# Kernel optimization log

Measured on AMD Instinct MI355X. Metric: run time of the kernel, lower is better.

The kernel has to match this reference:

```python
import jax, jax.numpy as jnp
import numpy as np
import math

K = 3          # wavelet order
ALPHA = 5      # fourier modes
LLEV = 0       # coarsest level
CVAL = 1       # channel multiplicity
K2 = K * K     # 9
B, NX, NY, T = 8, 64, 64, 64


def _linear(x, w, b):
    # torch nn.Linear: y = x @ W^T + b, W is [out, in]
    return jnp.einsum('...i,oi->...o', x, w) + b


def _wavelet_transform(x, ec_d, ec_s):
    # strided 4-way gather + concat along channel, then small matmuls
    xa = jnp.concatenate([x[:, ::2, ::2], x[:, ::2, 1::2],
                          x[:, 1::2, ::2], x[:, 1::2, 1::2]], axis=-1)
    return jnp.matmul(xa, ec_d), jnp.matmul(xa, ec_s)


def _even_odd(x, rc_ee, rc_eo, rc_oe, rc_oo):
    b, nx, ny, t, c, ich = x.shape
    k2 = ich // 2
    x_ee = jnp.matmul(x, rc_ee)
    x_eo = jnp.matmul(x, rc_eo)
    x_oe = jnp.matmul(x, rc_oe)
    x_oo = jnp.matmul(x, rc_oo)
    # interleave along Ny then Nx (equivalent to strided scatter into zeros)
    e = jnp.stack([x_ee, x_eo], axis=3).reshape(b, nx, 2 * ny, t, c, k2)
    o = jnp.stack([x_oe, x_oo], axis=3).reshape(b, nx, 2 * ny, t, c, k2)
    return jnp.stack([e, o], axis=2).reshape(b, 2 * nx, 2 * ny, t, c, k2)


def _kernel_ft(x, w1, w2, w3, w4, lo_w, lo_b):
    # sparseKernelFT3d
    b, nx, ny, t, c, ich = x.shape
    xr = x.reshape(b, nx, ny, t, c * ich).transpose(0, 4, 1, 2, 3)  # [B,C,Nx,Ny,T]
    xf = jnp.fft.rfftn(xr, axes=(-3, -2, -1))
    m = ALPHA
    l1 = min(m, nx // 2 + 1)
    l2 = min(m, ny // 2 + 1)
    cm = lambda a, w: jnp.einsum('bixyz,ioxyz->boxyz', a, w)
    w1c = w1[..., 0] + 1j * w1[..., 1]
    w2c = w2[..., 0] + 1j * w2[..., 1]
    w3c = w3[..., 0] + 1j * w3[..., 1]
    w4c = w4[..., 0] + 1j * w4[..., 1]
    out = jnp.zeros((b, c * ich, nx, ny, t // 2 + 1), dtype=xf.dtype)
    out = out.at[:, :, :l1, :l2, :m].set(cm(xf[:, :, :l1, :l2, :m], w1c[:, :, :l1, :l2, :]))
    out = out.at[:, :, nx - l1:, :l2, :m].set(cm(xf[:, :, nx - l1:, :l2, :m], w2c[:, :, :l1, :l2, :]))
    out = out.at[:, :, :l1, ny - l2:, :m].set(cm(xf[:, :, :l1, ny - l2:, :m], w3c[:, :, :l1, :l2, :]))
    out = out.at[:, :, nx - l1:, ny - l2:, :m].set(cm(xf[:, :, nx - l1:, ny - l2:, :m], w4c[:, :, :l1, :l2, :]))
    y = jnp.fft.irfftn(out, s=(nx, ny, t), axes=(-3, -2, -1))
    y = jax.nn.relu(y.transpose(0, 2, 3, 4, 1))
    y = _linear(y, lo_w, lo_b)
    return y.reshape(b, nx, ny, t, c, ich)


def _kernel_conv(x, cw, cb, lw, lb):
    # sparseKernel3d: conv3d(3,1,1) + ReLU, then Linear
    b, nx, ny, t, c, ich = x.shape
    xr = x.reshape(b, nx, ny, t, c * ich).transpose(0, 4, 1, 2, 3)
    y = jax.lax.conv_general_dilated(xr, cw, (1, 1, 1), 'SAME',
                                     dimension_numbers=('NCDHW', 'OIDHW', 'NCDHW'))
    y = jax.nn.relu(y + cb[None, :, None, None, None])
    y = _linear(y.transpose(0, 2, 3, 4, 1), lw, lb)
    return y.reshape(b, nx, ny, t, c, ich)


def setup_inputs() -> dict:
    key = jax.random.key(0)
    ks = jax.random.split(key, 24)
    r = lambda i, shp, s: jax.random.normal(ks[i], shp, dtype=jnp.float32) * s
    return {
        'x': r(0, (B, NX, NY, T, CVAL, K2), 1.0),
        'ec_s': r(1, (4 * K2, K2), 0.2), 'ec_d': r(2, (4 * K2, K2), 0.2),
        'rc_ee': r(3, (2 * K2, K2), 0.25), 'rc_eo': r(4, (2 * K2, K2), 0.25),
        'rc_oe': r(5, (2 * K2, K2), 0.25), 'rc_oo': r(6, (2 * K2, K2), 0.25),
        'w1': r(7, (K2, K2, ALPHA, ALPHA, ALPHA, 2), 0.05),
        'w2': r(8, (K2, K2, ALPHA, ALPHA, ALPHA, 2), 0.05),
        'w3': r(9, (K2, K2, ALPHA, ALPHA, ALPHA, 2), 0.05),
        'w4': r(10, (K2, K2, ALPHA, ALPHA, ALPHA, 2), 0.05),
        'A_Lo_w': r(11, (K2, K2), 0.2), 'A_Lo_b': r(12, (K2,), 0.1),
        'B_conv_w': r(13, (K2, K2, 3, 3, 3), 0.06), 'B_conv_b': r(14, (K2,), 0.1),
        'B_Lo_w': r(15, (K2, K2), 0.2), 'B_Lo_b': r(16, (K2,), 0.1),
        'C_conv_w': r(17, (K2, K2, 3, 3, 3), 0.06), 'C_conv_b': r(18, (K2,), 0.1),
        'C_Lo_w': r(19, (K2, K2), 0.2), 'C_Lo_b': r(20, (K2,), 0.1),
        'T0_w': r(21, (K2, K2), 0.2), 'T0_b': r(22, (K2,), 0.1),
    }


def reference(x, ec_s, ec_d, rc_ee, rc_eo, rc_oe, rc_oo, w1, w2, w3, w4,
              A_Lo_w, A_Lo_b, B_conv_w, B_conv_b, B_Lo_w, B_Lo_b,
              C_conv_w, C_conv_b, C_Lo_w, C_Lo_b, T0_w, T0_b):
    b, nx, ny, t, c, ich = x.shape
    ns = int(math.floor(math.log2(nx)))
    Ud, Us = [], []
    for _ in range(ns - LLEV):  # decompose
        d, x = _wavelet_transform(x, ec_d, ec_s)
        Ud.append(_kernel_ft(d, w1, w2, w3, w4, A_Lo_w, A_Lo_b)
                  + _kernel_conv(x, B_conv_w, B_conv_b, B_Lo_w, B_Lo_b))
        Us.append(_kernel_conv(d, C_conv_w, C_conv_b, C_Lo_w, C_Lo_b))
    n0 = 2 ** LLEV
    x = _linear(x.reshape(b, n0, n0, t, c * ich), T0_w, T0_b)
    x = x.reshape(b, n0, n0, t, c, ich)
    for i in range(ns - 1 - LLEV, -1, -1):  # reconstruct
        x = x + Us[i]
        x = jnp.concatenate([x, Ud[i]], axis=-1)
        x = _even_odd(x, rc_ee, rc_eo, rc_oe, rc_oo)
    return x
```

## Files before the change

kernel.cpp:

```cpp
#include <hip/hip_runtime.h>

#define TWO_PI 6.283185307179586f

struct Meta {
    int bz[7], by[7], bxm[7], bix[7], biz[7], bcv[7];
    int n[6], l1[6], L[6], NT[6];
    int soff[6];
    int tAo[6], tBo[6], tDo[6];
};

__device__ __forceinline__ int find_lev(const int* pre) {
    int lev = 0;
    #pragma unroll
    for (int i = 1; i < 6; ++i) lev += (int)(blockIdx.x >= (unsigned)pre[i]);
    return lev;
}


__global__ void wavelet_kernel(const float* __restrict__ x,
                               float* __restrict__ d, float* __restrict__ s,
                               const float* __restrict__ ec_d,
                               const float* __restrict__ ec_s,
                               int n, int total, int aos_in)
{
    __shared__ float wd[324], wsm[324];
    for (int i = threadIdx.x; i < 324; i += blockDim.x) { wd[i] = ec_d[i]; wsm[i] = ec_s[i]; }
    __syncthreads();
    int idx = blockIdx.x * blockDim.x + threadIdx.x;
    if (idx >= total) return;
    int it = idx & 63; int tmp = idx >> 6;
    int iy = tmp % n; tmp /= n;
    int ix = tmp % n; int b = tmp / n;
    int n2 = 2 * n;
    float a[36];
    if (aos_in) {
        const float* base = x + ((((size_t)(b * n2 + 2 * ix) * n2 + 2 * iy) * 64 + it) * 9);
        const float* p0 = base;
        const float* p1 = base + 576;
        const float* p2 = base + (size_t)n2 * 576;
        const float* p3 = p2 + 576;
        #pragma unroll
        for (int k = 0; k < 9; ++k) { a[k] = p0[k]; a[9+k] = p1[k]; a[18+k] = p2[k]; a[27+k] = p3[k]; }
    } else {
        const float* base = x + ((size_t)(b * n2 + 2 * ix) * n2 + 2 * iy) * 576 + it;
        const float* p0 = base;
        const float* p1 = base + 576;
        const float* p2 = base + (size_t)n2 * 576;
        const float* p3 = p2 + 576;
        #pragma unroll
        for (int k = 0; k < 9; ++k) { a[k] = p0[k*64]; a[9+k] = p1[k*64]; a[18+k] = p2[k*64]; a[27+k] = p3[k*64]; }
    }
    size_t ob = (size_t)(idx >> 6) * 576 + it;
    #pragma unroll
    for (int oc = 0; oc < 9; ++oc) {
        float vd = 0.f, vs = 0.f;
        #pragma unroll
        for (int k = 0; k < 36; ++k) { vd += a[k] * wd[k*9+oc]; vs += a[k] * wsm[k*9+oc]; }
        d[ob + oc*64] = vd; s[ob + oc*64] = vs;
    }
}

__global__ __launch_bounds__(256, 2)
void conv2_kernel(const float* __restrict__ s_all, float* __restrict__ ud_all,
                  const float* __restrict__ d_all, float* __restrict__ us_all,
                  const float* __restrict__ Bcw, const float* __restrict__ Bcb,
                  const float* __restrict__ Blw, const float* __restrict__ Blb,
                  const float* __restrict__ Ccw, const float* __restrict__ Ccb,
                  const float* __restrict__ Clw, const float* __restrict__ Clb,
                  Meta m)
{
    const int which = blockIdx.y;
    const float* cw = which ? Ccw : Bcw;
    const float* cb = which ? Ccb : Bcb;
    const float* lw = which ? Clw : Blw;
    const float* lb = which ? Clb : Blb;

    __shared__ float scw2[2430];
    __shared__ float slw[81], scb[9], slb[9];
    for (int i = threadIdx.x; i < 2187; i += 256) {
        int wo = i / 81, rem = i % 81, o = rem / 9, ic = rem % 9;
        scw2[(wo * 9 + o) * 10 + ic] = cw[(o * 9 + ic) * 27 + wo];
    }
    if (threadIdx.x < 81) slw[threadIdx.x] = lw[threadIdx.x];
    if (threadIdx.x < 9) { scb[threadIdx.x] = cb[threadIdx.x]; slb[threadIdx.x] = lb[threadIdx.x]; }
    __syncthreads();

    int lev = find_lev(m.bcv);
    int n = m.n[lev];
    int idx = (blockIdx.x - m.bcv[lev]) * 256 + threadIdx.x;
    int nh = (n + 1) >> 1;
    int total = 8 * n * nh * 64;
    if (idx >= total) return;
    int t = idx & 63; int tmp = idx >> 6;
    int iy0 = (tmp % nh) * 2; tmp /= nh;
    int ix = tmp % n; int b = tmp / n;
    bool has1 = (iy0 + 1) < n;
    const float* in = (which ? d_all : s_all) + (size_t)m.soff[lev] * 576;
    float* out      = (which ? us_all : ud_all) + (size_t)m.soff[lev] * 576;

    float acc0[9], acc1[9];
    #pragma unroll
    for (int o = 0; o < 9; ++o) { acc0[o] = scb[o]; acc1[o] = scb[o]; }

    for (int dd = 0; dd < 9; ++dd) {
        int dx = dd / 3 - 1, dt = dd % 3 - 1;
        int jx = ix + dx, jt = t + dt;
        bool okxt = ((unsigned)jx < (unsigned)n) && ((unsigned)jt < 64u);
        const float* rowbase = in + ((size_t)(b * n + (okxt ? jx : 0)) * n) * 576
                                  + (okxt ? jt : 0);
        float va[9], vb[9];
        {
            int jy = iy0 - 1; bool ok = okxt && (jy >= 0);
            const float* p = rowbase + (size_t)(ok ? jy : 0) * 576;
            #pragma unroll
            for (int ic = 0; ic < 9; ++ic) va[ic] = ok ? p[ic*64] : 0.f;
            const float* q = rowbase + (size_t)iy0 * 576;
            #pragma unroll
            for (int ic = 0; ic < 9; ++ic) vb[ic] = okxt ? q[ic*64] : 0.f;
        }
        #pragma unroll
        for (int k = 0; k < 3; ++k) {
            const float* wbase = &scw2[(((dx + 1) * 3 + k) * 3 + (dt + 1)) * 90];
            #pragma unroll
            for (int o = 0; o < 9; ++o) {
                const float* wp = wbase + o * 10;
                float2 w01 = *(const float2*)(wp);
                float2 w23 = *(const float2*)(wp + 2);
                float2 w45 = *(const float2*)(wp + 4);
                float2 w67 = *(const float2*)(wp + 6);
                float  w8  = wp[8];
                acc0[o] += va[0]*w01.x + va[1]*w01.y + va[2]*w23.x + va[3]*w23.y
                         + va[4]*w45.x + va[5]*w45.y + va[6]*w67.x + va[7]*w67.y + va[8]*w8;
                acc1[o] += vb[0]*w01.x + vb[1]*w01.y + vb[2]*w23.x + vb[3]*w23.y
                         + vb[4]*w45.x + vb[5]*w45.y + vb[6]*w67.x + vb[7]*w67.y + vb[8]*w8;
            }
            if (k < 2) {
                int jy = iy0 + k + 1; bool ok = okxt && (jy < n);
                const float* p = rowbase + (size_t)(ok ? jy : 0) * 576;
                #pragma unroll
                for (int ic = 0; ic < 9; ++ic) { va[ic] = vb[ic]; vb[ic] = ok ? p[ic*64] : 0.f; }
            }
        }
    }
    {
        float r[9];
        #pragma unroll
        for (int o = 0; o < 9; ++o) r[o] = fmaxf(acc0[o], 0.f);
        size_t ob = (size_t)((b * n + ix) * n + iy0) * 576 + t;
        #pragma unroll
        for (int o2 = 0; o2 < 9; ++o2) {
            float vv = slb[o2];
            #pragma unroll
            for (int o = 0; o < 9; ++o) vv += r[o] * slw[o2 * 9 + o];
            if (which == 0) out[ob + o2*64] += vv; else out[ob + o2*64] = vv;
        }
    }
    if (has1) {
        float r[9];
        #pragma unroll
        for (int o = 0; o < 9; ++o) r[o] = fmaxf(acc1[o], 0.f);
        size_t ob = (size_t)((b * n + ix) * n + iy0 + 1) * 576 + t;
        #pragma unroll
        for (int o2 = 0; o2 < 9; ++o2) {
            float vv = slb[o2];
            #pragma unroll
            for (int o = 0; o < 9; ++o) vv += r[o] * slw[o2 * 9 + o];
            if (which == 0) out[ob + o2*64] += vv; else out[ob + o2*64] = vv;
        }
    }
}

__global__ void fwdz_kernel(const float* __restrict__ d_all, float2* __restrict__ tA, Meta m)
{
    int lev = find_lev(m.bz);
    int n = m.n[lev];
    int idx = (blockIdx.x - m.bz[lev]) * 256 + threadIdx.x;
    int total = 8 * n * n * 45;
    if (idx >= total) return;
    int ic = idx % 9; int tmp = idx / 9;
    int kz = tmp % 5; int site = tmp / 5;
    const float* p = d_all + (size_t)(m.soff[lev] + site) * 576 + ic * 64;
    float re = 0.f, im = 0.f;
    for (int it = 0; it < 64; ++it) {
        int mm = (kz * it) & 63;
        float sv, cv; __sincosf((TWO_PI / 64.0f) * mm, &sv, &cv);
        float v = p[it];
        re += v * cv; im -= v * sv;
    }
    tA[m.tAo[lev] + idx] = make_float2(re, im);
}

__global__ void fwdy_kernel(const float2* __restrict__ tA, float2* __restrict__ tB, Meta m)
{
    int lev = find_lev(m.by);
    int n = m.n[lev], l1 = m.l1[lev], L = m.L[lev];
    int idx = (blockIdx.x - m.by[lev]) * 256 + threadIdx.x;
    int total = 8 * n * L * 45;
    if (idx >= total) return;
    int c45 = idx % 45; int tmp = idx / 45;
    int kyI = tmp % L; tmp /= L;
    int ix = tmp % n; int b = tmp / n;
    int ky = (kyI < l1) ? kyI : (n - L + kyI);
    const float2* p = tA + m.tAo[lev] + ((size_t)(b * n + ix) * n) * 45 + c45;
    float re = 0.f, im = 0.f;
    for (int iy = 0; iy < n; ++iy) {
        int mm = (ky * iy) & (n - 1);
        float sv, cv; __sincosf((TWO_PI / n) * mm, &sv, &cv);
        float2 a = p[(size_t)iy * 45];
        re += a.x * cv + a.y * sv;
        im += a.y * cv - a.x * sv;
    }
    tB[m.tBo[lev] + idx] = make_float2(re, im);
}

__global__ void fwdxmix_kernel(const float2* __restrict__ tB, float2* __restrict__ tD,
                               const float* __restrict__ w1, const float* __restrict__ w2,
                               const float* __restrict__ w3, const float* __restrict__ w4,
                               Meta m)
{
    __shared__ float2 sFzy[32 * 45];
    __shared__ float2 sF[10 * 45];
    int lev = find_lev(m.bxm);
    int n = m.n[lev], l1 = m.l1[lev], L = m.L[lev];
    int lb = blockIdx.x - m.bxm[lev];
    int kyI = lb % L;
    int b   = lb / L;
    int ky = (kyI < l1) ? kyI : (n - L + kyI);
    int nload = n * 45;
    for (int i = threadIdx.x; i < nload; i += blockDim.x) {
        int ix = i / 45, c = i % 45;
        sFzy[i] = tB[m.tBo[lev] + ((size_t)(b * n + ix) * L + kyI) * 45 + c];
    }
    __syncthreads();
    int nf = L * 45;
    for (int i = threadIdx.x; i < nf; i += blockDim.x) {
        int kxI = i / 45, c = i % 45;
        int kx = (kxI < l1) ? kxI : (n - L + kxI);
        float re = 0.f, im = 0.f;
        for (int ix = 0; ix < n; ++ix) {
            int mm = (kx * ix) & (n - 1);
            float sv, cv; __sincosf((TWO_PI / n) * mm, &sv, &cv);
            float2 a = sFzy[ix * 45 + c];
            re += a.x * cv + a.y * sv;
            im += a.y * cv - a.x * sv;
        }
        sF[i] = make_float2(re, im);
    }
    __syncthreads();
    bool ly = ky < l1, hy = ky >= n - l1;
    for (int i = threadIdx.x; i < nf; i += blockDim.x) {
        int kxI = i / 45, c = i % 45;
        int kz = c / 9, oc = c % 9;
        int kx = (kxI < l1) ? kxI : (n - L + kxI);
        bool lx = kx < l1, hx = kx >= n - l1;
        const float* w; int wx, wy;
        if (hx && hy)      { w = w4; wx = kx - (n - l1); wy = ky - (n - l1); }
        else if (lx && hy) { w = w3; wx = kx;            wy = ky - (n - l1); }
        else if (hx && ly) { w = w2; wx = kx - (n - l1); wy = ky; }
        else               { w = w1; wx = kx;            wy = ky; }
        const float* wb = w + (((size_t)oc * 5 + wx) * 5 + wy) * 10 + kz * 2;
        const float2* pf = &sF[kxI * 45 + kz * 9];
        float re = 0.f, im = 0.f;
        #pragma unroll
        for (int ic = 0; ic < 9; ++ic) {
            float2 a = pf[ic];
            float wr = wb[(size_t)ic * 2250];
            float wi = wb[(size_t)ic * 2250 + 1];
            re += a.x * wr - a.y * wi;
            im += a.x * wi + a.y * wr;
        }
        tD[m.tDo[lev] + (((size_t)(b * L + kxI) * L + kyI) * 5 + kz) * 9 + oc] = make_float2(re, im);
    }
}

__global__ void invx_kernel(const float2* __restrict__ tD, float2* __restrict__ tB, Meta m)
{
    int lev = find_lev(m.bix);
    int n = m.n[lev], l1 = m.l1[lev], L = m.L[lev];
    int idx = (blockIdx.x - m.bix[lev]) * 256 + threadIdx.x;
    int total = 8 * n * L * 45;
    if (idx >= total) return;
    int c45 = idx % 45; int tmp = idx / 45;
    int kyI = tmp % L; tmp /= L;
    int ix = tmp % n; int b = tmp / n;
    const float2* p = tD + m.tDo[lev] + ((size_t)b * L * L) * 45 + (size_t)kyI * 45 + c45;
    float re = 0.f, im = 0.f;
    for (int kxI = 0; kxI < L; ++kxI) {
        int kx = (kxI < l1) ? kxI : (n - L + kxI);
        int mm = (kx * ix) & (n - 1);
        float sv, cv; __sincosf((TWO_PI / n) * mm, &sv, &cv);
        float2 a = p[(size_t)kxI * L * 45];
        re += a.x * cv - a.y * sv;
        im += a.x * sv + a.y * cv;
    }
    tB[m.tBo[lev] + idx] = make_float2(re, im);
}

__global__ void invyz_kernel(const float2* __restrict__ tB, float* __restrict__ ud_all,
                             const float* __restrict__ lw, const float* __restrict__ lb,
                             Meta m)
{
    __shared__ float2 sG1[10 * 45];
    __shared__ float2 sG2[4 * 45];
    __shared__ float slw[81], slb[9];
    int lev = find_lev(m.biz);
    int n = m.n[lev], l1 = m.l1[lev], L = m.L[lev], NT = m.NT[lev];
    int TY = n / NT;
    int lb2 = blockIdx.x - m.biz[lev];
    int iyt = lb2 % NT;
    int ix  = (lb2 / NT) % n;
    int b   = lb2 / (NT * n);
    int iy0 = iyt * TY;
    if (threadIdx.x < 81) slw[threadIdx.x] = lw[threadIdx.x];
    if (threadIdx.x < 9)  slb[threadIdx.x] = lb[threadIdx.x];
    int nload = L * 45;
    for (int i = threadIdx.x; i < nload; i += blockDim.x)
        sG1[i] = tB[m.tBo[lev] + ((size_t)(b * n + ix) * L) * 45 + i];
    __syncthreads();
    int nf = TY * 45;
    for (int i = threadIdx.x; i < nf; i += blockDim.x) {
        int il = i / 45, c = i % 45;
        int iy = iy0 + il;
        float re = 0.f, im = 0.f;
        for (int kyI = 0; kyI < L; ++kyI) {
            int ky = (kyI < l1) ? kyI : (n - L + kyI);
            int mm = (ky * iy) & (n - 1);
            float sv, cv; __sincosf((TWO_PI / n) * mm, &sv, &cv);
            float2 a = sG1[kyI * 45 + c];
            re += a.x * cv - a.y * sv;
            im += a.x * sv + a.y * cv;
        }
        sG2[i] = make_float2(re, im);
    }
    __syncthreads();
    int t = threadIdx.x;
    if (t < TY * 64) {
        int il = t >> 6, it = t & 63;
        float inv_norm = 1.0f / ((float)n * (float)n * 64.0f);
        float cvz[5], svz[5];
        #pragma unroll
        for (int kz = 0; kz < 5; ++kz) {
            int mm = (kz * it) & 63;
            __sincosf((TWO_PI / 64.0f) * mm, &svz[kz], &cvz[kz]);
        }
        const float2* pg = &sG2[il * 45];
        float y[9];
        #pragma unroll
        for (int oc = 0; oc < 9; ++oc) {
            float v = 0.f;
            #pragma unroll
            for (int kz = 0; kz < 5; ++kz) {
                float2 a = pg[kz * 9 + oc];
                float term = a.x * cvz[kz] - a.y * svz[kz];
                v += (kz == 0 ? 1.0f : 2.0f) * term;
            }
            y[oc] = fmaxf(v * inv_norm, 0.f);
        }
        size_t ob = (size_t)(m.soff[lev] + (b * n + ix) * n + iy0 + il) * 576 + it;
        #pragma unroll
        for (int o2 = 0; o2 < 9; ++o2) {
            float v = slb[o2];
            #pragma unroll
            for (int oc = 0; oc < 9; ++oc) v += y[oc] * slw[o2 * 9 + oc];
            ud_all[ob + o2*64] = v;
        }
    }
}

__global__ void recon_kernel(const float* __restrict__ x, const float* __restrict__ Us,
                             const float* __restrict__ Ud, float* __restrict__ out,
                             const float* __restrict__ ree, const float* __restrict__ reo,
                             const float* __restrict__ roe, const float* __restrict__ roo,
                             const float* __restrict__ t0w, const float* __restrict__ t0b,
                             int n, int total, int apply_t0, int aos_out)
{
    __shared__ float s_m[4][162];
    __shared__ float st0[81], st0b[9];
    for (int i = threadIdx.x; i < 162; i += blockDim.x) {
        s_m[0][i] = ree[i]; s_m[1][i] = reo[i]; s_m[2][i] = roe[i]; s_m[3][i] = roo[i];
    }
    if (threadIdx.x < 81) st0[threadIdx.x] = t0w[threadIdx.x];
    if (threadIdx.x < 9)  st0b[threadIdx.x] = t0b[threadIdx.x];
    __syncthreads();
    int idx = blockIdx.x * blockDim.x + threadIdx.x;
    if (idx >= total) return;
    int it = idx & 63; int tmp = idx >> 6;
    int iy = tmp % n; tmp /= n;
    int ix = tmp % n; int b = tmp / n;
    float v[18];
    size_t ib = (size_t)(idx >> 6) * 576 + it;
    if (apply_t0) {
        float xr[9];
        #pragma unroll
        for (int k = 0; k < 9; ++k) xr[k] = x[ib + k*64];
        #pragma unroll
        for (int o = 0; o < 9; ++o) {
            float r = st0b[o];
            #pragma unroll
            for (int i = 0; i < 9; ++i) r += xr[i] * st0[o*9+i];
            v[o] = r + Us[ib + o*64];
        }
    } else {
        #pragma unroll
        for (int k = 0; k < 9; ++k) v[k] = x[ib + k*64] + Us[ib + k*64];
    }
    #pragma unroll
    for (int k = 0; k < 9; ++k) v[9+k] = Ud[ib + k*64];
    int n2 = 2 * n;
    #pragma unroll
    for (int q = 0; q < 4; ++q) {
        int rx = q >> 1, ry = q & 1;
        size_t site2 = ((size_t)(b * n2 + 2*ix + rx) * n2) + 2*iy + ry;
        const float* mm = s_m[q];
        if (aos_out) {
            size_t ob = (site2 * 64 + it) * 9;
            #pragma unroll
            for (int oc = 0; oc < 9; ++oc) {
                float r = 0.f;
                #pragma unroll
                for (int k = 0; k < 18; ++k) r += v[k] * mm[k*9+oc];
                out[ob + oc] = r;
            }
        } else {
            size_t ob = site2 * 576 + it;
            #pragma unroll
            for (int oc = 0; oc < 9; ++oc) {
                float r = 0.f;
                #pragma unroll
                for (int k = 0; k < 18; ++k) r += v[k] * mm[k*9+oc];
                out[ob + oc*64] = r;
            }
        }
    }
}

extern "C" void kernel_launch(void* const* d_in, const int* in_sizes, int n_in,
                              void* d_out, int out_size, void* d_ws, size_t ws_size,
                              hipStream_t stream)
{
    const float* x0    = (const float*)d_in[0];
    const float* ec_s  = (const float*)d_in[1];
    const float* ec_d  = (const float*)d_in[2];
    const float* rc_ee = (const float*)d_in[3];
    const float* rc_eo = (const float*)d_in[4];
    const float* rc_oe = (const float*)d_in[5];
    const float* rc_oo = (const float*)d_in[6];
    const float* w1    = (const float*)d_in[7];
    const float* w2    = (const float*)d_in[8];
    const float* w3    = (const float*)d_in[9];
    const float* w4    = (const float*)d_in[10];
    const float* A_Lo_w = (const float*)d_in[11];
    const float* A_Lo_b = (const float*)d_in[12];
    const float* B_cw  = (const float*)d_in[13];
    const float* B_cb  = (const float*)d_in[14];
    const float* B_lw  = (const float*)d_in[15];
    const float* B_lb  = (const float*)d_in[16];
    const float* C_cw  = (const float*)d_in[17];
    const float* C_cb  = (const float*)d_in[18];
    const float* C_lw  = (const float*)d_in[19];
    const float* C_lb  = (const float*)d_in[20];
    const float* T0_w  = (const float*)d_in[21];
    const float* T0_b  = (const float*)d_in[22];

    Meta m;
    int ns_[6] = {32, 16, 8, 4, 2, 1};
    int az = 0, ay = 0, axm = 0, aix = 0, aiz = 0, acv = 0;
    int aS = 0, aA = 0, aB = 0, aD = 0;
    for (int l = 0; l < 6; ++l) {
        int n = ns_[l];
        int l1 = (n / 2 + 1 < 5) ? (n / 2 + 1) : 5;
        int L = (2 * l1 < n) ? 2 * l1 : n;
        int TY = (n < 4) ? n : 4;
        int NT = n / TY;
        int nh = (n + 1) / 2;
        m.n[l] = n; m.l1[l] = l1; m.L[l] = L; m.NT[l] = NT;
        m.soff[l] = aS; m.tAo[l] = aA; m.tBo[l] = aB; m.tDo[l] = aD;
        m.bz[l] = az; m.by[l] = ay; m.bxm[l] = axm; m.bix[l] = aix; m.biz[l] = aiz; m.bcv[l] = acv;
        az  += (8 * n * n * 45 + 255) / 256;
        ay  += (8 * n * L * 45 + 255) / 256;
        axm += 8 * L;
        aix += (8 * n * L * 45 + 255) / 256;
        aiz += 8 * n * NT;
        acv += (8 * n * nh * 64 + 255) / 256;
        aS += 8 * n * n; aA += 8 * n * n * 45; aB += 8 * n * L * 45; aD += 8 * L * L * 45;
    }
    m.bz[6] = az; m.by[6] = ay; m.bxm[6] = axm; m.bix[6] = aix; m.biz[6] = aiz; m.bcv[6] = acv;

    float* ws = (float*)d_ws;
    size_t off = 0;
    auto alloc = [&](size_t nf) { float* p = ws + off; off += (nf + 3) & ~(size_t)3; return p; };
    size_t NSf = (size_t)aS * 576;
    float* d_all  = alloc(NSf);
    float* s_all  = alloc(NSf);
    float* ud_all = alloc(NSf);
    float* us_all = alloc(NSf);
    float2* tA = (float2*)alloc((size_t)aA * 2);
    float2* tB = (float2*)alloc((size_t)aB * 2);
    float2* tD = (float2*)alloc((size_t)aD * 2);
    float* pingA = alloc((size_t)8 * 32 * 32 * 64 * 9);
    float* pingB = alloc((size_t)8 * 16 * 16 * 64 * 9);

    const int BLK = 256;

    for (int lev = 0; lev < 6; ++lev) {
        int n = ns_[lev];
        const float* xin = (lev == 0) ? x0 : (s_all + (size_t)m.soff[lev-1] * 576);
        int total = 8 * n * n * 64;
        wavelet_kernel<<<(total + BLK - 1) / BLK, BLK, 0, stream>>>(
            xin, d_all + (size_t)m.soff[lev] * 576, s_all + (size_t)m.soff[lev] * 576,
            ec_d, ec_s, n, total, (lev == 0) ? 1 : 0);
    }

    fwdz_kernel  <<<az,  BLK, 0, stream>>>(d_all, tA, m);
    fwdy_kernel  <<<ay,  BLK, 0, stream>>>(tA, tB, m);
    fwdxmix_kernel<<<axm, BLK, 0, stream>>>(tB, tD, w1, w2, w3, w4, m);
    invx_kernel  <<<aix, BLK, 0, stream>>>(tD, tB, m);
    invyz_kernel <<<aiz, BLK, 0, stream>>>(tB, ud_all, A_Lo_w, A_Lo_b, m);
    dim3 cgrid(acv, 2);
    conv2_kernel <<<cgrid, BLK, 0, stream>>>(s_all, ud_all, d_all, us_all,
                                             B_cw, B_cb, B_lw, B_lb,
                                             C_cw, C_cb, C_lw, C_lb, m);

    float* cur = nullptr;
    for (int lev = 5; lev >= 0; --lev) {
        int n = ns_[lev];
        int total = 8 * n * n * 64;
        const float* xin = (lev == 5) ? (s_all + (size_t)m.soff[5] * 576) : cur;
        float* outp = (lev == 0) ? (float*)d_out : ((lev & 1) ? pingA : pingB);
        recon_kernel<<<(total + BLK - 1) / BLK, BLK, 0, stream>>>(
            xin, us_all + (size_t)m.soff[lev] * 576, ud_all + (size_t)m.soff[lev] * 576, outp,
            rc_ee, rc_eo, rc_oe, rc_oo, T0_w, T0_b, n, total,
            (lev == 5) ? 1 : 0, (lev == 0) ? 1 : 0);
        cur = outp;
    }
}
```

Before: 651.2 us.

## Share time-neighbour conv inputs via wavefront shuffles and stage fwd-z DFT input in LDS

The 3D conv kernel now loads each (x,y) input column once per thread and gets the t-1 and t+1 values from neighbouring lanes with shuffles, instead of issuing separate global loads for each time offset. This cuts global loads roughly threefold, and the weights are re-laid out so all three time taps sit together per output channel. The forward z-DFT kernel now stages four sites' data in padded shared memory so reads are coalesced, at the cost of leaving 76 of 256 threads idle in the compute phase. The shuffle approach relies on t mapping to consecutive lanes across 64 lanes, which holds with wave64.

New measurement: 2.226 ms. 242% more time.

```diff
diff --git a/kernel.cpp b/kernel.cpp
--- a/kernel.cpp
+++ b/kernel.cpp
@@ -75,11 +75,13 @@
     const float* lw = which ? Clw : Blw;
     const float* lb = which ? Clb : Blb;
 
-    __shared__ float scw2[2430];
+    __shared__ float scw[2592];
     __shared__ float slw[81], scb[9], slb[9];
     for (int i = threadIdx.x; i < 2187; i += 256) {
-        int wo = i / 81, rem = i % 81, o = rem / 9, ic = rem % 9;
-        scw2[(wo * 9 + o) * 10 + ic] = cw[(o * 9 + ic) * 27 + wo];
+        int ic = i % 9; int r1 = i / 9;
+        int dt = r1 % 3; int r2 = r1 / 3;
+        int o = r2 % 9; int dxy = r2 / 9;
+        scw[(dxy * 9 + o) * 32 + dt * 10 + ic] = cw[(o * 9 + ic) * 27 + dxy * 3 + dt];
     }
     if (threadIdx.x < 81) slw[threadIdx.x] = lw[threadIdx.x];
     if (threadIdx.x < 9) { scb[threadIdx.x] = cb[threadIdx.x]; slb[threadIdx.x] = lb[threadIdx.x]; }
@@ -102,43 +104,59 @@
     #pragma unroll
     for (int o = 0; o < 9; ++o) { acc0[o] = scb[o]; acc1[o] = scb[o]; }
 
-    for (int dd = 0; dd < 9; ++dd) {
-        int dx = dd / 3 - 1, dt = dd % 3 - 1;
-        int jx = ix + dx, jt = t + dt;
-        bool okxt = ((unsigned)jx < (unsigned)n) && ((unsigned)jt < 64u);
-        const float* rowbase = in + ((size_t)(b * n + (okxt ? jx : 0)) * n) * 576
-                                  + (okxt ? jt : 0);
-        float va[9], vb[9];
+    for (int dx = -1; dx <= 1; ++dx) {
+        int jx = ix + dx; bool okx = (unsigned)jx < (unsigned)n;
+        const float* colbase = in + ((size_t)(b * n + (okx ? jx : 0)) * n) * 576 + t;
+        float A0[9], Am[9], Ap[9], B0[9], Bm[9], Bp[9];
         {
-            int jy = iy0 - 1; bool ok = okxt && (jy >= 0);
-            const float* p = rowbase + (size_t)(ok ? jy : 0) * 576;
-            #pragma unroll
-            for (int ic = 0; ic < 9; ++ic) va[ic] = ok ? p[ic*64] : 0.f;
-            const float* q = rowbase + (size_t)iy0 * 576;
-            #pragma unroll
-            for (int ic = 0; ic < 9; ++ic) vb[ic] = okxt ? q[ic*64] : 0.f;
-        }
-        #pragma unroll
-        for (int k = 0; k < 3; ++k) {
-            const float* wbase = &scw2[(((dx + 1) * 3 + k) * 3 + (dt + 1)) * 90];
+            int jy = iy0 - 1; bool ok = okx && (jy >= 0);
+            const float* p = colbase + (size_t)(ok ? jy : 0) * 576;
+            #pragma unroll
+            for (int ic = 0; ic < 9; ++ic) A0[ic] = ok ? p[ic*64] : 0.f;
+            const float* q = colbase + (size_t)iy0 * 576;
+            #pragma unroll
+            for (int ic = 0; ic < 9; ++ic) B0[ic] = okx ? q[ic*64] : 0.f;
+        }
+        #pragma unroll
+        for (int ic = 0; ic < 9; ++ic) {
+            float u1 = __shfl_up(A0[ic], 1);   Am[ic] = (t == 0)  ? 0.f : u1;
+            float d1 = __shfl_down(A0[ic], 1); Ap[ic] = (t == 63) ? 0.f : d1;
+            float u2 = __shfl_up(B0[ic], 1);   Bm[ic] = (t == 0)  ? 0.f : u2;
+            float d2 = __shfl_down(B0[ic], 1); Bp[ic] = (t == 63) ? 0.f : d2;
+        }
+        #pragma unroll
+        for (int dy = 0; dy < 3; ++dy) {
+            const float* wb2 = &scw[((dx + 1) * 3 + dy) * 288];
             #pragma unroll
             for (int o = 0; o < 9; ++o) {
-                const float* wp = wbase + o * 10;
-                float2 w01 = *(const float2*)(wp);
-                float2 w23 = *(const float2*)(wp + 2);
-                float2 w45 = *(const float2*)(wp + 4);
-                float2 w67 = *(const float2*)(wp + 6);
-                float  w8  = wp[8];
-                acc0[o] += va[0]*w01.x + va[1]*w01.y + va[2]*w23.x + va[3]*w23.y
-                         + va[4]*w45.x + va[5]*w45.y + va[6]*w67.x + va[7]*w67.y + va[8]*w8;
-                acc1[o] += vb[0]*w01.x + vb[1]*w01.y + vb[2]*w23.x + vb[3]*w23.y
-                         + vb[4]*w45.x + vb[5]*w45.y + vb[6]*w67.x + vb[7]*w67.y + vb[8]*w8;
+                const float* wp = wb2 + o * 32;
+                float sa = 0.f, sb = 0.f;
+                #pragma unroll
+                for (int ic = 0; ic < 8; ic += 2) {
+                    float2 wm = *(const float2*)(wp + ic);
+                    float2 w0 = *(const float2*)(wp + 10 + ic);
+                    float2 wq = *(const float2*)(wp + 20 + ic);
+                    sa += Am[ic]*wm.x + Am[ic+1]*wm.y + A0[ic]*w0.x + A0[ic+1]*w0.y
+                        + Ap[ic]*wq.x + Ap[ic+1]*wq.y;
+                    sb += Bm[ic]*wm.x + Bm[ic+1]*wm.y + B0[ic]*w0.x + B0[ic+1]*w0.y
+                        + Bp[ic]*wq.x + Bp[ic+1]*wq.y;
+                }
+                sa += Am[8]*wp[8] + A0[8]*wp[18] + Ap[8]*wp[28];
+                sb += Bm[8]*wp[8] + B0[8]*wp[18] + Bp[8]*wp[28];
+                acc0[o] += sa; acc1[o] += sb;
             }
-            if (k < 2) {
-                int jy = iy0 + k + 1; bool ok = okxt && (jy < n);
-                const float* p = rowbase + (size_t)(ok ? jy : 0) * 576;
+            if (dy < 2) {
                 #pragma unroll
-                for (int ic = 0; ic < 9; ++ic) { va[ic] = vb[ic]; vb[ic] = ok ? p[ic*64] : 0.f; }
+                for (int ic = 0; ic < 9; ++ic) { A0[ic]=B0[ic]; Am[ic]=Bm[ic]; Ap[ic]=Bp[ic]; }
+                int jy = iy0 + dy + 1; bool ok = okx && (jy < n);
+                const float* p = colbase + (size_t)(ok ? jy : 0) * 576;
+                #pragma unroll
+                for (int ic = 0; ic < 9; ++ic) B0[ic] = ok ? p[ic*64] : 0.f;
+                #pragma unroll
+                for (int ic = 0; ic < 9; ++ic) {
+                    float u2 = __shfl_up(B0[ic], 1);   Bm[ic] = (t == 0)  ? 0.f : u2;
+                    float d2 = __shfl_down(B0[ic], 1); Bp[ic] = (t == 63) ? 0.f : d2;
+                }
             }
         }
     }
@@ -172,22 +190,31 @@
 
 __global__ void fwdz_kernel(const float* __restrict__ d_all, float2* __restrict__ tA, Meta m)
 {
+    __shared__ float sd[4 * 600];
     int lev = find_lev(m.bz);
-    int n = m.n[lev];
-    int idx = (blockIdx.x - m.bz[lev]) * 256 + threadIdx.x;
-    int total = 8 * n * n * 45;
-    if (idx >= total) return;
-    int ic = idx % 9; int tmp = idx / 9;
-    int kz = tmp % 5; int site = tmp / 5;
-    const float* p = d_all + (size_t)(m.soff[lev] + site) * 576 + ic * 64;
-    float re = 0.f, im = 0.f;
-    for (int it = 0; it < 64; ++it) {
-        int mm = (kz * it) & 63;
-        float sv, cv; __sincosf((TWO_PI / 64.0f) * mm, &sv, &cv);
-        float v = p[it];
-        re += v * cv; im -= v * sv;
-    }
-    tA[m.tAo[lev] + idx] = make_float2(re, im);
+    int blk = blockIdx.x - m.bz[lev];
+    int s0 = blk * 4;
+    const float* src = d_all + ((size_t)m.soff[lev] + s0) * 576;
+    for (int i = threadIdx.x; i < 4 * 576; i += 256) {
+        int s = i / 576, r = i % 576;
+        int oc = r >> 6, it = r & 63;
+        sd[s * 600 + oc * 66 + it] = src[i];
+    }
+    __syncthreads();
+    int tid = threadIdx.x;
+    if (tid < 180) {
+        int s = tid / 45, c = tid % 45;
+        int kz = c / 9, ic = c % 9;
+        const float* p = &sd[s * 600 + ic * 66];
+        float re = 0.f, im = 0.f;
+        for (int it = 0; it < 64; ++it) {
+            int mm = (kz * it) & 63;
+            float sv, cv; __sincosf((TWO_PI / 64.0f) * mm, &sv, &cv);
+            float v = p[it];
+            re += v * cv; im -= v * sv;
+        }
+        tA[m.tAo[lev] + (size_t)(s0 + s) * 45 + c] = make_float2(re, im);
+    }
 }
 
 __global__ void fwdy_kernel(const float2* __restrict__ tA, float2* __restrict__ tB, Meta m)
@@ -476,7 +503,7 @@
         m.n[l] = n; m.l1[l] = l1; m.L[l] = L; m.NT[l] = NT;
         m.soff[l] = aS; m.tAo[l] = aA; m.tBo[l] = aB; m.tDo[l] = aD;
         m.bz[l] = az; m.by[l] = ay; m.bxm[l] = axm; m.bix[l] = aix; m.biz[l] = aiz; m.bcv[l] = acv;
-        az  += (8 * n * n * 45 + 255) / 256;
+        az  += (8 * n * n) / 4;
         ay  += (8 * n * L * 45 + 255) / 256;
         axm += 8 * L;
         aix += (8 * n * L * 45 + 255) / 256;
```
